# Performance work log

Measured on AMD Instinct MI355X. Metric: run time of the kernel, lower is better.

The kernel has to match this reference:

```python
import jax, jax.numpy as jnp
import numpy as np

N_NODES = 100000
N_EDGES = 1200000
D = 64


def gcn_conv(x, src, dst, ew, W, b, n):
    # add self-loops with weight 1 (PyG GCNConv default)
    loops = jnp.arange(n)
    s = jnp.concatenate([src, loops])
    d = jnp.concatenate([dst, loops])
    w = jnp.concatenate([ew, jnp.ones((n,), ew.dtype)])
    deg = jax.ops.segment_sum(w, d, num_segments=n)           # [n]
    dis = jnp.where(deg > 0, jax.lax.rsqrt(deg), 0.0)
    norm = dis[s] * w * dis[d]                                # [E+n]
    h = x @ W                                                 # [n, out]
    msg = norm[:, None] * h[s]                                # gather
    out = jax.ops.segment_sum(msg, d, num_segments=n)         # scatter
    return out + b


def setup_inputs() -> dict:
    key = jax.random.key(0)
    ks = jax.random.split(key, 7)
    x = jax.random.normal(ks[0], (N_NODES, D), dtype=jnp.float32)
    edge_index = jax.random.randint(ks[1], (2, N_EDGES), 0, N_NODES, dtype=jnp.int64)
    edge_weight = jax.random.uniform(ks[2], (N_EDGES,), dtype=jnp.float32)
    W1 = jax.random.normal(ks[3], (D, D), dtype=jnp.float32) * (1.0 / np.sqrt(D))
    b1 = jnp.zeros((D,), dtype=jnp.float32)
    W2 = jax.random.normal(ks[4], (D, D), dtype=jnp.float32) * (1.0 / np.sqrt(D))
    b2 = jnp.zeros((D,), dtype=jnp.float32)
    return {"x": x, "edge_index": edge_index, "edge_weight": edge_weight,
            "W1": W1, "b1": b1, "W2": W2, "b2": b2}


def reference(x, edge_index, edge_weight, W1, b1, W2, b2):
    n = x.shape[0]
    src, dst = edge_index[0], edge_index[1]
    x1 = jax.nn.relu(gcn_conv(x, src, dst, edge_weight, W1, b1, n))
    x2 = jax.nn.relu(gcn_conv(x1, src, dst, edge_weight, W2, b2, n))
    return (x1 + x2) * 0.5
```

## Files before the change

### kernel.cpp

```cpp
#include <hip/hip_runtime.h>

#define NN 100000
#define NE 1200000
#define DD 64
#define NBUCK 196
#define BCAP 7168
#define TILE 4096
#define NB1 293
#define NB_G 1563
#define FIX25 33554432.0f
#define FIX25_INV (1.0f/33554432.0f)

typedef short bf16x8 __attribute__((ext_vector_type(8)));
typedef float f32x4  __attribute__((ext_vector_type(4)));

static __device__ __forceinline__ unsigned short f2bf(float f) {
    unsigned int u = __float_as_uint(f);
    unsigned int r = (u + 0x7fffu + ((u >> 16) & 1u)) >> 16;
    return (unsigned short)r;
}
static __device__ __forceinline__ float bf2f(unsigned short s) {
    return __uint_as_float(((unsigned int)s) << 16);
}


__global__ __launch_bounds__(256) void prep(
    int* __restrict__ cursor,
    const float* __restrict__ W1, const float* __restrict__ W2,
    unsigned short* __restrict__ Wt1, unsigned short* __restrict__ Wt2)
{
    if (blockIdx.x == 0) {
        if (threadIdx.x < NBUCK) cursor[threadIdx.x] = 0;
        return;
    }
    const float* W = (blockIdx.x == 1) ? W1 : W2;
    unsigned short* Wt = (blockIdx.x == 1) ? Wt1 : Wt2;
    int t = threadIdx.x;
    int col = t >> 2, k0 = (t & 3) * 16;
    #pragma unroll
    for (int i = 0; i < 16; ++i)
        Wt[col * 64 + k0 + i] = f2bf(W[(k0 + i) * 64 + col]);
}


static __device__ __forceinline__ void gemm_body(
    const float* __restrict__ x, const unsigned short* __restrict__ Wt,
    unsigned short* __restrict__ h16, int r0, int t,
    unsigned short* Xs, unsigned short* Ws)
{
    {
        int col = t >> 2, seg = (t & 3) * 16;
        const uint4* p = (const uint4*)(Wt + col * 64 + seg);
        uint4 a0 = p[0], a1 = p[1];
        *(uint4*)&Ws[col * 72 + seg]     = a0;
        *(uint4*)&Ws[col * 72 + seg + 8] = a1;
    }
    {
        int row = t >> 2, seg = (t & 3) * 16;
        int gr = r0 + row;
        float4 v0 = {0,0,0,0}, v1 = v0, v2 = v0, v3 = v0;
        if (gr < NN) {
            const float4* p = (const float4*)(x + (size_t)gr * DD + seg);
            v0 = p[0]; v1 = p[1]; v2 = p[2]; v3 = p[3];
        }
        ushort4 h0 = { f2bf(v0.x), f2bf(v0.y), f2bf(v0.z), f2bf(v0.w) };
        ushort4 h1 = { f2bf(v1.x), f2bf(v1.y), f2bf(v1.z), f2bf(v1.w) };
        ushort4 h2 = { f2bf(v2.x), f2bf(v2.y), f2bf(v2.z), f2bf(v2.w) };
        ushort4 h3 = { f2bf(v3.x), f2bf(v3.y), f2bf(v3.z), f2bf(v3.w) };
        *(ushort4*)&Xs[row * 72 + seg]      = h0;
        *(ushort4*)&Xs[row * 72 + seg + 4]  = h1;
        *(ushort4*)&Xs[row * 72 + seg + 8]  = h2;
        *(ushort4*)&Xs[row * 72 + seg + 12] = h3;
    }
    __syncthreads();

    const int wv = t >> 6;
    const int ln = t & 63;
    const int m  = ln & 15;
    const int q  = ln >> 4;
    const int arow = wv * 16 + m;

    bf16x8 a0 = *(const bf16x8*)&Xs[arow * 72 + q * 8];
    bf16x8 a1 = *(const bf16x8*)&Xs[arow * 72 + 32 + q * 8];

    f32x4 acc[4];
    #pragma unroll
    for (int c = 0; c < 4; ++c) {
        bf16x8 b0 = *(const bf16x8*)&Ws[(c * 16 + m) * 72 + q * 8];
        bf16x8 b1 = *(const bf16x8*)&Ws[(c * 16 + m) * 72 + 32 + q * 8];
        f32x4 z = {0.f, 0.f, 0.f, 0.f};
        z = __builtin_amdgcn_mfma_f32_16x16x32_bf16(a0, b0, z, 0, 0, 0);
        z = __builtin_amdgcn_mfma_f32_16x16x32_bf16(a1, b1, z, 0, 0, 0);
        acc[c] = z;
    }

    #pragma unroll
    for (int r = 0; r < 4; ++r) {
        int grow = r0 + wv * 16 + q * 4 + r;
        if (grow < NN) {
            #pragma unroll
            for (int c = 0; c < 4; ++c)
                h16[(size_t)grow * DD + c * 16 + m] = f2bf(acc[c][r]);
        }
    }
}


__global__ __launch_bounds__(256) void pass1_gemm(
    const int* __restrict__ src, const int* __restrict__ dst,
    const float* __restrict__ ew, int* __restrict__ cursor,
    unsigned long long* __restrict__ stage,
    const float* __restrict__ x, const unsigned short* __restrict__ Wt1,
    unsigned short* __restrict__ h16)
{
    __shared__ unsigned short Xs[64 * 72];
    __shared__ unsigned short Ws[64 * 72];
    __shared__ int cnt[NBUCK];
    __shared__ int resv[NBUCK];

    const int t = threadIdx.x;

    if (blockIdx.x >= NB1) {
        gemm_body(x, Wt1, h16, (blockIdx.x - NB1) * 64, t, Xs, Ws);
        return;
    }

    const int base = blockIdx.x * TILE;
    if (t < NBUCK) cnt[t] = 0;
    __syncthreads();

    #pragma unroll
    for (int k = 0; k < TILE / 256; ++k) {
        int e = base + k * 256 + t;
        if (e < NE) atomicAdd(&cnt[dst[e] >> 9], 1);
    }
    __syncthreads();
    if (t < NBUCK) {
        int c = cnt[t];
        resv[t] = c ? atomicAdd(&cursor[t], c) : 0;
        cnt[t] = 0;
    }
    __syncthreads();
    #pragma unroll
    for (int k = 0; k < TILE / 256; ++k) {
        int e = base + k * 256 + t;
        if (e < NE) {
            int d = dst[e];
            int b = d >> 9;
            int r = atomicAdd(&cnt[b], 1);
            int pos = resv[b] + r;
            if (pos < BCAP) {
                unsigned int meta = ((unsigned int)(d & 511) << 17) |
                                    (unsigned int)src[e];
                stage[(size_t)b * BCAP + pos] =
                    ((unsigned long long)meta << 32) | __float_as_uint(ew[e]);
            }
        }
    }
}


__global__ __launch_bounds__(512) void pass2(
    const unsigned long long* __restrict__ stage, const int* __restrict__ cursor,
    unsigned int* __restrict__ slots, unsigned int* __restrict__ degdis)
{
    __shared__ int cnt[512];
    __shared__ unsigned sum[512];

    const int b = blockIdx.x;
    const int t = threadIdx.x;
    const int n0 = b << 9;
    const int cntb = min(cursor[b], BCAP);

    cnt[t] = 0; sum[t] = 0;
    __syncthreads();

    for (int k = t; k < cntb; k += 512) {
        unsigned long long E = stage[(size_t)b * BCAP + k];
        unsigned int meta = (unsigned int)(E >> 32);
        int dl = meta >> 17;
        float w = __uint_as_float((unsigned int)E);
        int r = atomicAdd(&cnt[dl], 1);
        atomicAdd(&sum[dl], (unsigned)(w * FIX25));
        if (r < 63)
            slots[(size_t)(n0 + dl) * 64 + r] =
                ((meta & 0x1ffffu) << 15) | (f2bf(w) & 0x7fffu);
    }
    __syncthreads();

    int node = n0 + t;
    if (node < NN) {
        float deg = 1.0f + (float)sum[t] * FIX25_INV;
        float di = rsqrtf(deg);
        degdis[node] = (__float_as_uint(di) & ~63u) |
                       (unsigned)min(cnt[t], 63);
    }
}


template <bool FINAL>
__global__ __launch_bounds__(256) void gather(
    const unsigned short* __restrict__ h16, const float* __restrict__ bias,
    const unsigned int* __restrict__ degdis, const unsigned int* __restrict__ slots,
    const float* __restrict__ prev, float* __restrict__ out)
{
    const int node = __builtin_amdgcn_readfirstlane(
        (blockIdx.x * blockDim.x + threadIdx.x) >> 6);
    const int lane = threadIdx.x & 63;
    if (node >= NN) return;

    const int g = lane >> 4;
    const int l = lane & 15;
    const int l4 = l << 2;

    const unsigned int* seg = slots + (size_t)node * 64;

    const unsigned int dd = degdis[node];
    const int deg = dd & 63;
    const float di = __uint_as_float(dd & ~63u);

    const ushort4 hs = *(const ushort4*)(h16 + (size_t)node * DD + l4);
    const float4  bb = *(const float4*)(bias + l4);
    float4 p = {0.f, 0.f, 0.f, 0.f};
    if (FINAL) p = *(const float4*)(prev + (size_t)node * DD + l4);

    f32x4 acc0 = {0,0,0,0}, acc1 = {0,0,0,0}, acc2 = {0,0,0,0}, acc3 = {0,0,0,0};

#define QUADX(q, joff, rq, nq)                                                 \
    {                                                                          \
        unsigned w0 = seg[(joff) + 4*q + 0], w1 = seg[(joff) + 4*q + 1];       \
        unsigned w2 = seg[(joff) + 4*q + 2], w3 = seg[(joff) + 4*q + 3];       \
        unsigned ea = (g & 1) ? w1 : w0;                                       \
        unsigned eb = (g & 1) ? w3 : w2;                                       \
        unsigned e  = (g & 2) ? eb : ea;                                       \
        unsigned srow = e >> 15;                                               \
        srow = (srow < NN) ? srow : 0u;                                        \
        float dsrc = __uint_as_float(degdis[srow] & ~63u);                     \
        rq = *(const ushort4*)(h16 + ((size_t)srow << 6) + l4);                \
        float nv_ = bf2f((unsigned short)(e & 0x7fffu)) * di * dsrc;           \
        nq = ((joff) + 4*q + g < deg) ? nv_ : 0.f;                             \
    }
#define FMA4(rq, nq, ac)                                                       \
    ac[0] = fmaf(nq, bf2f(rq.x), ac[0]);                                       \
    ac[1] = fmaf(nq, bf2f(rq.y), ac[1]);                                       \
    ac[2] = fmaf(nq, bf2f(rq.z), ac[2]);                                       \
    ac[3] = fmaf(nq, bf2f(rq.w), ac[3]);

    {
        ushort4 r0, r1, r2, r3;
        float n0, n1, n2, n3;
        QUADX(0, 0, r0, n0)
        QUADX(1, 0, r1, n1)
        QUADX(2, 0, r2, n2)
        QUADX(3, 0, r3, n3)
        FMA4(r0, n0, acc0)
        FMA4(r1, n1, acc1)
        FMA4(r2, n2, acc2)
        FMA4(r3, n3, acc3)
    }
    if (deg > 16) {
        for (int j = 16; j < deg; j += 16) {
            ushort4 r0, r1, r2, r3;
            float n0, n1, n2, n3;
            QUADX(0, j, r0, n0)
            QUADX(1, j, r1, n1)
            QUADX(2, j, r2, n2)
            QUADX(3, j, r3, n3)
            FMA4(r0, n0, acc0)
            FMA4(r1, n1, acc1)
            FMA4(r2, n2, acc2)
            FMA4(r3, n3, acc3)
        }
    }
#undef QUADX
#undef FMA4

    float s0 = (acc0[0] + acc1[0]) + (acc2[0] + acc3[0]);
    float s1 = (acc0[1] + acc1[1]) + (acc2[1] + acc3[1]);
    float s2 = (acc0[2] + acc1[2]) + (acc2[2] + acc3[2]);
    float s3 = (acc0[3] + acc1[3]) + (acc2[3] + acc3[3]);

    s0 += __shfl_xor(s0, 16); s1 += __shfl_xor(s1, 16);
    s2 += __shfl_xor(s2, 16); s3 += __shfl_xor(s3, 16);
    s0 += __shfl_xor(s0, 32); s1 += __shfl_xor(s1, 32);
    s2 += __shfl_xor(s2, 32); s3 += __shfl_xor(s3, 32);

    if (g == 0) {
        const float dsq = di * di;
        float v0 = fmaxf(fmaf(dsq, bf2f(hs.x), bb.x) + s0, 0.f);
        float v1 = fmaxf(fmaf(dsq, bf2f(hs.y), bb.y) + s1, 0.f);
        float v2 = fmaxf(fmaf(dsq, bf2f(hs.z), bb.z) + s2, 0.f);
        float v3 = fmaxf(fmaf(dsq, bf2f(hs.w), bb.w) + s3, 0.f);
        float4 o;
        if (FINAL) {
            o.x = 0.5f * (p.x + v0); o.y = 0.5f * (p.y + v1);
            o.z = 0.5f * (p.z + v2); o.w = 0.5f * (p.w + v3);
        } else {
            o.x = v0; o.y = v1; o.z = v2; o.w = v3;
        }
        *(float4*)(out + (size_t)node * DD + l4) = o;
    }
}

__global__ __launch_bounds__(256) void gemm_mfma(
    const float* __restrict__ x, const unsigned short* __restrict__ Wt,
    unsigned short* __restrict__ h16)
{
    __shared__ unsigned short Xs[64 * 72];
    __shared__ unsigned short Ws[64 * 72];
    gemm_body(x, Wt, h16, blockIdx.x * 64, threadIdx.x, Xs, Ws);
}


extern "C" void kernel_launch(void* const* d_in, const int* in_sizes, int n_in,
                              void* d_out, int out_size, void* d_ws, size_t ws_size,
                              hipStream_t stream) {
    const float* x   = (const float*)d_in[0];
    const int*   ei  = (const int*)d_in[1];
    const float* ewt = (const float*)d_in[2];
    const float* W1  = (const float*)d_in[3];
    const float* b1  = (const float*)d_in[4];
    const float* W2  = (const float*)d_in[5];
    const float* b2  = (const float*)d_in[6];
    float* out = (float*)d_out;

    const int* srcv = ei;
    const int* dstv = ei + NE;

    float* wsf = (float*)d_ws;
    int* cursor = (int*)wsf;
    unsigned short* Wt1 = (unsigned short*)(wsf + 256);
    unsigned short* Wt2 = Wt1 + 4096;
    unsigned int* degdis = (unsigned int*)(wsf + 4352);
    unsigned long long* stage = (unsigned long long*)(wsf + 104448);
    unsigned int* slots = (unsigned int*)(wsf + 104448 + 2 * NBUCK * BCAP);
    unsigned short* h16 = (unsigned short*)(slots + (size_t)NN * 64);

    const int GB = (NN * 64) / 256;

    prep<<<3, 256, 0, stream>>>(cursor, W1, W2, Wt1, Wt2);
    pass1_gemm<<<NB1 + NB_G, 256, 0, stream>>>(srcv, dstv, ewt, cursor, stage,
                                               x, Wt1, h16);
    pass2<<<NBUCK, 512, 0, stream>>>(stage, cursor, slots, degdis);

    gather<false><<<GB, 256, 0, stream>>>(h16, b1, degdis, slots, nullptr, out);
    gemm_mfma<<<NB_G, 256, 0, stream>>>(out, Wt2, h16);
    gather<true><<<GB, 256, 0, stream>>>(h16, b2, degdis, slots, out, out);
}
```

Baseline: 195.4 us.

## Drop prep kernel, convert weights inline, zero slots in pass1, widen gather prologue

Removes the separate prep kernel: each GEMM block now reads W from fp32 and converts it to bf16 itself, and the cursor reset becomes a memset. Extra blocks appended to pass1 zero the slots array, and the gather's first iteration now covers 32 edges instead of 16 before falling into the loop. The aim is fewer launches and more memory-level parallelism in the gather. In exchange, every GEMM block does redundant strided fp32 weight loads and conversions, and pass1 has to write the full slots buffer.

Result: slower. 215.4 us (+10.2%).

```diff
diff --git a/kernel.cpp b/kernel.cpp
--- a/kernel.cpp
+++ b/kernel.cpp
@@ -8,6 +8,7 @@
 #define TILE 4096
 #define NB1 293
 #define NB_G 1563
+#define NZS 391
 #define FIX25 33554432.0f
 #define FIX25_INV (1.0f/33554432.0f)
 
@@ -24,36 +25,19 @@
 }
 
 
-__global__ __launch_bounds__(256) void prep(
-    int* __restrict__ cursor,
-    const float* __restrict__ W1, const float* __restrict__ W2,
-    unsigned short* __restrict__ Wt1, unsigned short* __restrict__ Wt2)
-{
-    if (blockIdx.x == 0) {
-        if (threadIdx.x < NBUCK) cursor[threadIdx.x] = 0;
-        return;
-    }
-    const float* W = (blockIdx.x == 1) ? W1 : W2;
-    unsigned short* Wt = (blockIdx.x == 1) ? Wt1 : Wt2;
-    int t = threadIdx.x;
-    int col = t >> 2, k0 = (t & 3) * 16;
-    #pragma unroll
-    for (int i = 0; i < 16; ++i)
-        Wt[col * 64 + k0 + i] = f2bf(W[(k0 + i) * 64 + col]);
-}
-
-
 static __device__ __forceinline__ void gemm_body(
-    const float* __restrict__ x, const unsigned short* __restrict__ Wt,
+    const float* __restrict__ x, const float* __restrict__ W,
     unsigned short* __restrict__ h16, int r0, int t,
     unsigned short* Xs, unsigned short* Ws)
 {
     {
         int col = t >> 2, seg = (t & 3) * 16;
-        const uint4* p = (const uint4*)(Wt + col * 64 + seg);
-        uint4 a0 = p[0], a1 = p[1];
-        *(uint4*)&Ws[col * 72 + seg]     = a0;
-        *(uint4*)&Ws[col * 72 + seg + 8] = a1;
+        unsigned short tmp[16];
+        #pragma unroll
+        for (int i = 0; i < 16; ++i)
+            tmp[i] = f2bf(W[(size_t)(seg + i) * 64 + col]);
+        *(uint4*)&Ws[col * 72 + seg]     = *(uint4*)&tmp[0];
+        *(uint4*)&Ws[col * 72 + seg + 8] = *(uint4*)&tmp[8];
     }
     {
         int row = t >> 2, seg = (t & 3) * 16;
@@ -109,8 +93,8 @@
 __global__ __launch_bounds__(256) void pass1_gemm(
     const int* __restrict__ src, const int* __restrict__ dst,
     const float* __restrict__ ew, int* __restrict__ cursor,
-    unsigned long long* __restrict__ stage,
-    const float* __restrict__ x, const unsigned short* __restrict__ Wt1,
+    unsigned long long* __restrict__ stage, unsigned int* __restrict__ slots,
+    const float* __restrict__ x, const float* __restrict__ W1,
     unsigned short* __restrict__ h16)
 {
     __shared__ unsigned short Xs[64 * 72];
@@ -120,8 +104,22 @@
 
     const int t = threadIdx.x;
 
+    if (blockIdx.x >= NB1 + NB_G) {
+        const int zb = blockIdx.x - (NB1 + NB_G);
+        uint4* sl = (uint4*)slots;
+        const size_t total = (size_t)NN * 16;
+        size_t base = (size_t)zb * 4096 + t;
+        const uint4 z = {0u, 0u, 0u, 0u};
+        #pragma unroll
+        for (int i = 0; i < 16; ++i) {
+            size_t idx = base + (size_t)i * 256;
+            if (idx < total) sl[idx] = z;
+        }
+        return;
+    }
+
     if (blockIdx.x >= NB1) {
-        gemm_body(x, Wt1, h16, (blockIdx.x - NB1) * 64, t, Xs, Ws);
+        gemm_body(x, W1, h16, (blockIdx.x - NB1) * 64, t, Xs, Ws);
         return;
     }
 
@@ -247,19 +245,27 @@
     ac[3] = fmaf(nq, bf2f(rq.w), ac[3]);
 
     {
-        ushort4 r0, r1, r2, r3;
-        float n0, n1, n2, n3;
+        ushort4 r0, r1, r2, r3, r4, r5, r6, r7;
+        float n0, n1, n2, n3, n4, n5, n6, n7;
         QUADX(0, 0, r0, n0)
         QUADX(1, 0, r1, n1)
         QUADX(2, 0, r2, n2)
         QUADX(3, 0, r3, n3)
+        QUADX(4, 0, r4, n4)
+        QUADX(5, 0, r5, n5)
+        QUADX(6, 0, r6, n6)
+        QUADX(7, 0, r7, n7)
         FMA4(r0, n0, acc0)
         FMA4(r1, n1, acc1)
         FMA4(r2, n2, acc2)
         FMA4(r3, n3, acc3)
-    }
-    if (deg > 16) {
-        for (int j = 16; j < deg; j += 16) {
+        FMA4(r4, n4, acc0)
+        FMA4(r5, n5, acc1)
+        FMA4(r6, n6, acc2)
+        FMA4(r7, n7, acc3)
+    }
+    if (deg > 32) {
+        for (int j = 32; j < deg; j += 16) {
             ushort4 r0, r1, r2, r3;
             float n0, n1, n2, n3;
             QUADX(0, j, r0, n0)
@@ -303,12 +309,12 @@
 }
 
 __global__ __launch_bounds__(256) void gemm_mfma(
-    const float* __restrict__ x, const unsigned short* __restrict__ Wt,
+    const float* __restrict__ x, const float* __restrict__ W,
     unsigned short* __restrict__ h16)
 {
     __shared__ unsigned short Xs[64 * 72];
     __shared__ unsigned short Ws[64 * 72];
-    gemm_body(x, Wt, h16, blockIdx.x * 64, threadIdx.x, Xs, Ws);
+    gemm_body(x, W, h16, blockIdx.x * 64, threadIdx.x, Xs, Ws);
 }
 
 
@@ -329,8 +335,6 @@
 
     float* wsf = (float*)d_ws;
     int* cursor = (int*)wsf;
-    unsigned short* Wt1 = (unsigned short*)(wsf + 256);
-    unsigned short* Wt2 = Wt1 + 4096;
     unsigned int* degdis = (unsigned int*)(wsf + 4352);
     unsigned long long* stage = (unsigned long long*)(wsf + 104448);
     unsigned int* slots = (unsigned int*)(wsf + 104448 + 2 * NBUCK * BCAP);
@@ -338,12 +342,12 @@
 
     const int GB = (NN * 64) / 256;
 
-    prep<<<3, 256, 0, stream>>>(cursor, W1, W2, Wt1, Wt2);
-    pass1_gemm<<<NB1 + NB_G, 256, 0, stream>>>(srcv, dstv, ewt, cursor, stage,
-                                               x, Wt1, h16);
+    hipMemsetAsync(cursor, 0, NBUCK * sizeof(int), stream);
+    pass1_gemm<<<NB1 + NB_G + NZS, 256, 0, stream>>>(srcv, dstv, ewt, cursor,
+                                                     stage, slots, x, W1, h16);
     pass2<<<NBUCK, 512, 0, stream>>>(stage, cursor, slots, degdis);
 
     gather<false><<<GB, 256, 0, stream>>>(h16, b1, degdis, slots, nullptr, out);
-    gemm_mfma<<<NB_G, 256, 0, stream>>>(out, Wt2, h16);
+    gemm_mfma<<<NB_G, 256, 0, stream>>>(out, W2, h16);
     gather<true><<<GB, 256, 0, stream>>>(h16, b2, degdis, slots, out, out);
 }
```
